# Performance work log

Hardware: AMD Instinct MI355X
Metric: run time of the kernel (lower is better)

Reference implementation:

```python
import jax, jax.numpy as jnp
import numpy as np

D_MODEL = 1024
N_HEADS = 16
HEAD_DIM = D_MODEL // N_HEADS  # 64
WINDOW = 15
NUM_RANDOM = 2
B, L = 2, 2048


def setup_inputs() -> dict:
    key = jax.random.key(0)
    ks = jax.random.split(key, 5)
    x = jax.random.normal(ks[0], (B, L, D_MODEL), dtype=jnp.float32)
    # rotary angles: theta[t, j] = t / 10000^(2j/head_dim), shape [1, L, head_dim//2]
    inv_freq = 1.0 / (10000.0 ** (jnp.arange(0, HEAD_DIM, 2, dtype=jnp.float32) / HEAD_DIM))
    t = jnp.arange(L, dtype=jnp.float32)
    freqs = (t[:, None] * inv_freq[None, :])[None].astype(jnp.float32)  # [1,L,32]
    scale = 0.02
    wq = jax.random.normal(ks[1], (D_MODEL, D_MODEL), dtype=jnp.float32) * scale
    wk = jax.random.normal(ks[2], (D_MODEL, D_MODEL), dtype=jnp.float32) * scale
    wv = jax.random.normal(ks[3], (D_MODEL, D_MODEL), dtype=jnp.float32) * scale
    wo = jax.random.normal(ks[4], (D_MODEL, D_MODEL), dtype=jnp.float32) * scale
    return {"x": x, "freqs": freqs, "wq": wq, "wk": wk, "wv": wv, "wo": wo}


def _rope(t, cos, sin):
    # t: [B,H,L,hd]; interpret last dim as (hd/2, 2) complex pairs and rotate.
    tr = t.reshape(*t.shape[:-1], -1, 2)
    re, im = tr[..., 0], tr[..., 1]
    out_re = re * cos - im * sin
    out_im = re * sin + im * cos
    return jnp.stack([out_re, out_im], axis=-1).reshape(t.shape)


def _bigbird_mask(Lq):
    ii = jnp.arange(Lq)[:, None]
    jj = jnp.arange(Lq)[None, :]
    causal = jj <= ii
    window = jnp.abs(ii - jj) <= (WINDOW // 2)
    glob = (ii == 0) | (jj == 0)
    # random mask: per row i, NUM_RANDOM indices uniform in [0, i]
    rkey = jax.random.key(42)
    u = jax.random.uniform(rkey, (Lq, NUM_RANDOM))
    ridx = jnp.floor(u * (jnp.arange(Lq, dtype=jnp.float32)[:, None] + 1.0)).astype(jnp.int32)
    rmask = jnp.zeros((Lq, Lq), dtype=bool).at[jnp.arange(Lq)[:, None], ridx].set(True)
    # rows with <= NUM_RANDOM causal options attend to all of them
    rmask = rmask | (causal & (ii < NUM_RANDOM))
    return (causal & (window | rmask)) | glob  # [L,L]


def reference(x, freqs, wq, wk, wv, wo):
    b, l, _ = x.shape
    q = (x @ wq.T).reshape(b, l, N_HEADS, HEAD_DIM).transpose(0, 2, 1, 3)  # [B,H,L,hd]
    k = (x @ wk.T).reshape(b, l, N_HEADS, HEAD_DIM).transpose(0, 2, 1, 3)
    v = (x @ wv.T).reshape(b, l, N_HEADS, HEAD_DIM).transpose(0, 2, 1, 3)
    cos = jnp.cos(freqs[:, :l])[:, None]  # [1,1,L,hd/2]
    sin = jnp.sin(freqs[:, :l])[:, None]
    q = _rope(q, cos, sin)
    k = _rope(k, cos, sin)
    attn_mask = _bigbird_mask(l)  # [L,L], broadcast over B,H
    scale = 1.0 / jnp.sqrt(jnp.float32(HEAD_DIM))
    scores = jnp.einsum("bhqd,bhkd->bhqk", q, k) * scale
    scores = jnp.where(attn_mask[None, None], scores, jnp.finfo(scores.dtype).min)
    p = jax.nn.softmax(scores, axis=-1)
    out = jnp.einsum("bhqk,bhkd->bhqd", p, v)
    out = out.transpose(0, 2, 1, 3).reshape(b, l, D_MODEL)
    return out @ wo.T
```

## Files before the change

kernel.cpp:

```cpp
#include <hip/hip_runtime.h>
#include <math.h>

#define SEQ_L 2048
#define DM 1024
#define NH 16
#define HD 64
#define NB 2
#define KD 1024
#define ND 1024

typedef __bf16 bf16;
typedef __bf16 bf16x8 __attribute__((ext_vector_type(8)));
typedef __bf16 bf16x4 __attribute__((ext_vector_type(4)));
typedef float f32x4 __attribute__((ext_vector_type(4)));

__device__ inline uint32_t rotl32(uint32_t v, int n) { return (v << n) | (v >> (32 - n)); }

__device__ inline void threefry(uint32_t x0, uint32_t x1, uint32_t* o0, uint32_t* o1) {
  const uint32_t ks0 = 0u, ks1 = 42u, ks2 = 0u ^ 42u ^ 0x1BD11BDAu;
  x0 += ks0; x1 += ks1;
#define TF_R(rr) { x0 += x1; x1 = rotl32(x1, rr); x1 ^= x0; }
  TF_R(13) TF_R(15) TF_R(26) TF_R(6)
  x0 += ks1; x1 += ks2 + 1u;
  TF_R(17) TF_R(29) TF_R(16) TF_R(24)
  x0 += ks2; x1 += ks0 + 2u;
  TF_R(13) TF_R(15) TF_R(26) TF_R(6)
  x0 += ks0; x1 += ks1 + 3u;
  TF_R(17) TF_R(29) TF_R(16) TF_R(24)
  x0 += ks1; x1 += ks2 + 4u;
  TF_R(13) TF_R(15) TF_R(26) TF_R(6)
  x0 += ks2; x1 += ks0 + 5u;
#undef TF_R
  *o0 = x0; *o1 = x1;
}

__device__ inline int rand_col(int i, int s) {
  uint32_t o0, o1;
  threefry(0u, (uint32_t)(2 * i + s), &o0, &o1);
  uint32_t bits = o0 ^ o1;
  float u = __uint_as_float((bits >> 9) | 0x3f800000u) - 1.0f;
  return (int)floorf(u * (float)(i + 1));
}

__global__ void prep_kernel(const float* __restrict__ x,
                            const float* __restrict__ w0, const float* __restrict__ w1,
                            const float* __restrict__ w2, const float* __restrict__ w3,
                            const float* __restrict__ freqs,
                            bf16* __restrict__ xb,
                            bf16* __restrict__ o0, bf16* __restrict__ o1,
                            bf16* __restrict__ o2, bf16* __restrict__ o3,
                            int* __restrict__ ctab, float2* __restrict__ rtab) {
  const int bx = blockIdx.x;
  const int t = threadIdx.x;
  if (bx < 8192) {
    const float* src;
    bf16* dst;
    int idx;
    if (bx < 4096) { src = x; dst = xb; idx = bx * 256 + t; }
    else {
      int widx = bx - 4096;
      int wsel = widx >> 10;
      switch (wsel) {
        case 0: src = w0; dst = o0; break;
        case 1: src = w1; dst = o1; break;
        case 2: src = w2; dst = o2; break;
        default: src = w3; dst = o3; break;
      }
      idx = (widx & 1023) * 256 + t;
    }
    float4 vv = ((const float4*)src)[idx];
    bf16x4 ov;
    ov[0] = (bf16)vv.x; ov[1] = (bf16)vv.y; ov[2] = (bf16)vv.z; ov[3] = (bf16)vv.w;
    *(bf16x4*)(dst + (size_t)idx * 4) = ov;
    return;
  }
  if (bx < 8200) {
    const int i = (bx - 8192) * 256 + t;
    int cols[11]; int nc = 0;
    if (i >= 1) {
      int lo = i - 7; if (lo < 0) lo = 0;
      for (int j = lo; j <= i; ++j) cols[nc++] = j;
      if (lo > 0) cols[nc++] = 0;
#pragma unroll
      for (int s = 0; s < 2; ++s) {
        int rj = rand_col(i, s);
        bool dup = false;
        for (int c2 = 0; c2 < nc; ++c2) dup |= (cols[c2] == rj);
        if (!dup) cols[nc++] = rj;
      }
    }
    for (int c2 = nc; c2 < 11; ++c2) cols[c2] = -1;
#pragma unroll
    for (int c2 = 0; c2 < 11; ++c2) ctab[i * 12 + c2] = cols[c2];
    ctab[i * 12 + 11] = nc;
    return;
  }
  const int idx = (bx - 8200) * 256 + t;
  float s, c;
  sincosf(freqs[idx], &s, &c);
  rtab[idx] = make_float2(c, s);
}

__device__ inline void gld16(const bf16* g, bf16* l) {
  __builtin_amdgcn_global_load_lds((const __attribute__((address_space(1))) void*)g,
                                   (__attribute__((address_space(3))) void*)l, 16, 0, 0);
}

template <typename OutT>
__device__ inline void gemm_bt_body(const bf16* __restrict__ A, const bf16* __restrict__ W,
                                    OutT* __restrict__ C, const float2* __restrict__ rtab) {
  __shared__ __align__(16) bf16 As[128 * 32];
  __shared__ __align__(16) bf16 Bs[128 * 32];
  const int t = threadIdx.x;
  const int lane = t & 63;
  const int wave = t >> 6;
  const int wm = (wave >> 1) * 64;
  const int wn = (wave & 1) * 64;
  const int m0 = blockIdx.x * 128;
  const int n0 = blockIdx.y * 128;
  const int r = t >> 2;
  const int ck = (t & 3) * 8;
  const int l15 = lane & 15;
  const int koff = (lane >> 4) * 8;

  f32x4 acc[4][4] = {};

  for (int k0 = 0; k0 < KD; k0 += 32) {
    gld16(A + (size_t)(m0 + r) * KD + k0 + ck, As + t * 8);
    gld16(A + (size_t)(m0 + 64 + r) * KD + k0 + ck, As + 2048 + t * 8);
    gld16(W + (size_t)(n0 + r) * KD + k0 + ck, Bs + t * 8);
    gld16(W + (size_t)(n0 + 64 + r) * KD + k0 + ck, Bs + 2048 + t * 8);
    __syncthreads();
    bf16x8 af[4], bfr[4];
#pragma unroll
    for (int mt = 0; mt < 4; ++mt)
      af[mt] = *(const bf16x8*)(As + (wm + mt * 16 + l15) * 32 + koff);
#pragma unroll
    for (int nt = 0; nt < 4; ++nt)
      bfr[nt] = *(const bf16x8*)(Bs + (wn + nt * 16 + l15) * 32 + koff);
#pragma unroll
    for (int mt = 0; mt < 4; ++mt)
#pragma unroll
      for (int nt = 0; nt < 4; ++nt)
        acc[mt][nt] = __builtin_amdgcn_mfma_f32_16x16x32_bf16(af[mt], bfr[nt], acc[mt][nt], 0, 0, 0);
    __syncthreads();
  }
  const int colb = n0 + wn + l15;
  const int rowb = m0 + wm + (lane >> 4) * 4;
  const int odd = l15 & 1;
#pragma unroll
  for (int mt = 0; mt < 4; ++mt)
#pragma unroll
    for (int nt = 0; nt < 4; ++nt) {
      const int col = colb + nt * 16;
      const int jj = (col & 63) >> 1;
#pragma unroll
      for (int rr = 0; rr < 4; ++rr) {
        float val = acc[mt][nt][rr];
        if (rtab) {
          const int row = rowb + mt * 16 + rr;
          const int l = row & (SEQ_L - 1);
          float2 cs = rtab[l * 32 + jj];
          float partner = __shfl_xor(val, 1);
          val = odd ? val * cs.x + partner * cs.y : val * cs.x - partner * cs.y;
        }
        C[(size_t)(rowb + mt * 16 + rr) * ND + colb + nt * 16] = (OutT)val;
      }
    }
}

__global__ __launch_bounds__(256, 3) void qkv_gemm_kernel(
    const bf16* __restrict__ xb, const bf16* __restrict__ wqb, const bf16* __restrict__ wkb,
    const bf16* __restrict__ wvb, bf16* __restrict__ qb, bf16* __restrict__ kb, bf16* __restrict__ vb,
    const float2* __restrict__ rtab) {
  const bf16* W = blockIdx.z == 0 ? wqb : blockIdx.z == 1 ? wkb : wvb;
  bf16* O = blockIdx.z == 0 ? qb : blockIdx.z == 1 ? kb : vb;
  const float2* rt = blockIdx.z < 2 ? rtab : nullptr;
  gemm_bt_body<bf16>(xb, W, O, rt);
}

__global__ __launch_bounds__(256, 2) void out_gemm_kernel(
    bf16* __restrict__ ab, const bf16* __restrict__ wob, float* __restrict__ out,
    const float* __restrict__ pm, const float* __restrict__ pz, const float* __restrict__ pv) {
  const int t = threadIdx.x;
  const int m0 = blockIdx.x * 64;
  const int n0 = blockIdx.y * 128;

  if (blockIdx.x == 0 || blockIdx.x == 32) {
    const int b = blockIdx.x == 0 ? 0 : 1;
#pragma unroll
    for (int e = t; e < DM; e += 256) {
      const int h = e >> 6, d = e & 63;
      const int base = b * 128 + h * 8;
      float M = -1e30f;
#pragma unroll
      for (int c = 0; c < 8; ++c) M = fmaxf(M, pm[base + c]);
      float Z = 0.f, od = 0.f;
#pragma unroll
      for (int c = 0; c < 8; ++c) {
        float sc = __expf(pm[base + c] - M);
        Z += pz[base + c] * sc;
        od += pv[(base + c) * 64 + d] * sc;
      }
      ab[(size_t)b * SEQ_L * DM + e] = (bf16)(od / Z);
    }
    __syncthreads();
  }

  __shared__ __align__(16) bf16 As[64 * 32];
  __shared__ __align__(16) bf16 Bs[128 * 32];
  const int lane = t & 63;
  const int wave = t >> 6;
  const int wm = (wave >> 1) * 32;
  const int wn = (wave & 1) * 64;
  const int r = t >> 2;
  const int ck = (t & 3) * 8;
  const int l15 = lane & 15;
  const int koff = (lane >> 4) * 8;

  f32x4 acc[2][4] = {};

  for (int k0 = 0; k0 < KD; k0 += 32) {
    gld16(ab + (size_t)(m0 + r) * KD + k0 + ck, As + t * 8);
    gld16(wob + (size_t)(n0 + r) * KD + k0 + ck, Bs + t * 8);
    gld16(wob + (size_t)(n0 + 64 + r) * KD + k0 + ck, Bs + 2048 + t * 8);
    __syncthreads();
    bf16x8 af[2], bfr[4];
#pragma unroll
    for (int mt = 0; mt < 2; ++mt)
      af[mt] = *(const bf16x8*)(As + (wm + mt * 16 + l15) * 32 + koff);
#pragma unroll
    for (int nt = 0; nt < 4; ++nt)
      bfr[nt] = *(const bf16x8*)(Bs + (wn + nt * 16 + l15) * 32 + koff);
#pragma unroll
    for (int mt = 0; mt < 2; ++mt)
#pragma unroll
      for (int nt = 0; nt < 4; ++nt)
        acc[mt][nt] = __builtin_amdgcn_mfma_f32_16x16x32_bf16(af[mt], bfr[nt], acc[mt][nt], 0, 0, 0);
    __syncthreads();
  }
  const int colb = n0 + wn + l15;
  const int rowb = m0 + wm + (lane >> 4) * 4;
#pragma unroll
  for (int mt = 0; mt < 2; ++mt)
#pragma unroll
    for (int nt = 0; nt < 4; ++nt)
#pragma unroll
      for (int rr = 0; rr < 4; ++rr)
        out[(size_t)(rowb + mt * 16 + rr) * ND + colb + nt * 16] = acc[mt][nt][rr];
}

__global__ __launch_bounds__(256) void attn_kernel(const bf16* __restrict__ q, const bf16* __restrict__ k,
                                                   const bf16* __restrict__ v, bf16* __restrict__ o,
                                                   const int* __restrict__ ctab,
                                                   float* __restrict__ pm, float* __restrict__ pz,
                                                   float* __restrict__ pv) {
  const int t = threadIdx.x;
  const int lane = t & 63;
  const int w = t >> 6;

  __shared__ float sbuf[256];
  __shared__ float redm[4], redz[4];
  __shared__ float part[4][64];

  if (blockIdx.x < 1024) {
    const int b = blockIdx.x >> 9;
    const int tt = blockIdx.x & 511;
    const int tile = ((tt & 7) << 6) + (tt >> 3);
    const int i = tile * 4 + 1 + w;
    if (i >= SEQ_L) return;
    const size_t bb = (size_t)b * SEQ_L * DM;
    const int eo = lane * 16;

    const bf16* qrow = q + bb + (size_t)i * DM + eo;
    bf16x8 qv0 = *(const bf16x8*)(qrow);
    bf16x8 qv1 = *(const bf16x8*)(qrow + 8);

    const int4* cp = (const int4*)(ctab + i * 12);
    int4 ca = cp[0], cb = cp[1], cc = cp[2];
    int cols[11] = {ca.x, ca.y, ca.z, ca.w, cb.x, cb.y, cb.z, cb.w, cc.x, cc.y, cc.z};

    float sv[11];
#pragma unroll
    for (int c = 0; c < 11; ++c) {
      int cj = cols[c] < 0 ? 0 : cols[c];
      const bf16* krow = k + bb + (size_t)cj * DM + eo;
      bf16x8 kv0 = *(const bf16x8*)(krow);
      bf16x8 kv1 = *(const bf16x8*)(krow + 8);
      float acc = 0.f;
#pragma unroll
      for (int e = 0; e < 8; ++e)
        acc += (float)qv0[e] * (float)kv0[e] + (float)qv1[e] * (float)kv1[e];
      sv[c] = acc;
    }
#pragma unroll
    for (int c = 0; c < 11; ++c) {
      sv[c] += __shfl_xor(sv[c], 1);
      sv[c] += __shfl_xor(sv[c], 2);
      sv[c] = cols[c] < 0 ? -1e30f : sv[c] * 0.125f;
    }
    float m = -1e30f;
#pragma unroll
    for (int c = 0; c < 11; ++c) m = fmaxf(m, sv[c]);
    float z = 0.f;
#pragma unroll
    for (int c = 0; c < 11; ++c) { sv[c] = __expf(sv[c] - m); z += sv[c]; }
    const float inv = 1.f / z;

    float oa[16] = {};
#pragma unroll
    for (int c = 0; c < 11; ++c) {
      int cj = cols[c] < 0 ? 0 : cols[c];
      const bf16* vrow = v + bb + (size_t)cj * DM + eo;
      bf16x8 vv0 = *(const bf16x8*)(vrow);
      bf16x8 vv1 = *(const bf16x8*)(vrow + 8);
#pragma unroll
      for (int e = 0; e < 8; ++e) {
        oa[e]     += sv[c] * (float)vv0[e];
        oa[8 + e] += sv[c] * (float)vv1[e];
      }
    }
    bf16x8 ov0, ov1;
#pragma unroll
    for (int e = 0; e < 8; ++e) {
      ov0[e] = (bf16)(oa[e] * inv);
      ov1[e] = (bf16)(oa[8 + e] * inv);
    }
    bf16* orow = o + bb + (size_t)i * DM + eo;
    *(bf16x8*)(orow) = ov0;
    *(bf16x8*)(orow + 8) = ov1;
    return;
  }

  const int idx = blockIdx.x - 1024;
  const int b = idx >> 7;
  const int rem = idx & 127;
  const int h = rem >> 3;
  const int c = rem & 7;
  const size_t hb = (size_t)b * SEQ_L * DM + (size_t)h * HD;
  const int j = c * 256 + t;

  bf16x8 qv8[8];
#pragma unroll
  for (int cc = 0; cc < 8; ++cc) qv8[cc] = *(const bf16x8*)(q + hb + cc * 8);

  float acc = 0.f;
#pragma unroll
  for (int cc = 0; cc < 8; ++cc) {
    bf16x8 kv = *(const bf16x8*)(k + hb + (size_t)j * DM + cc * 8);
#pragma unroll
    for (int e = 0; e < 8; ++e) acc += (float)qv8[cc][e] * (float)kv[e];
  }
  float s = acc * 0.125f;
  float mloc = s;
#pragma unroll
  for (int off = 32; off > 0; off >>= 1) mloc = fmaxf(mloc, __shfl_xor(mloc, off));
  if (lane == 0) redm[w] = mloc;
  __syncthreads();
  const float m = fmaxf(fmaxf(redm[0], redm[1]), fmaxf(redm[2], redm[3]));

  float e = __expf(s - m);
  sbuf[t] = e;
  float zloc = e;
#pragma unroll
  for (int off = 32; off > 0; off >>= 1) zloc += __shfl_xor(zloc, off);
  if (lane == 0) redz[w] = zloc;
  __syncthreads();
  const float zc = redz[0] + redz[1] + redz[2] + redz[3];

  float oa = 0.f;
  for (int jj = w; jj < 256; jj += 4)
    oa += sbuf[jj] * (float)v[hb + (size_t)(c * 256 + jj) * DM + lane];
  part[w][lane] = oa;
  __syncthreads();
  if (t < 64) pv[idx * 64 + t] = part[0][t] + part[1][t] + part[2][t] + part[3][t];
  if (t == 0) { pm[idx] = m; pz[idx] = zc; }
}

extern "C" void kernel_launch(void* const* d_in, const int* in_sizes, int n_in,
                              void* d_out, int out_size, void* d_ws, size_t ws_size,
                              hipStream_t stream) {
  const float* x     = (const float*)d_in[0];
  const float* freqs = (const float*)d_in[1];
  const float* wq    = (const float*)d_in[2];
  const float* wk    = (const float*)d_in[3];
  const float* wv    = (const float*)d_in[4];
  const float* wo    = (const float*)d_in[5];
  float* out = (float*)d_out;

  char* ws = (char*)d_ws;
  bf16* xb  = (bf16*)(ws + 0);
  bf16* wqb = (bf16*)(ws + 8388608);
  bf16* wkb = (bf16*)(ws + 10485760);
  bf16* wvb = (bf16*)(ws + 12582912);
  bf16* wob = (bf16*)(ws + 14680064);
  bf16* qb  = (bf16*)(ws + 16777216);
  bf16* kb  = (bf16*)(ws + 25165824);
  bf16* vb  = (bf16*)(ws + 33554432);
  bf16* ab  = (bf16*)(ws + 41943040);
  int*    ctab = (int*)(ws + 50331648);
  float*  pm   = (float*)(ws + 50462720);
  float*  pz   = (float*)(ws + 50463744);
  float*  pv   = (float*)(ws + 50464768);
  float2* rtab = (float2*)(ws + 50593792);
  (void)ws_size;

  prep_kernel<<<8456, 256, 0, stream>>>(x, wq, wk, wv, wo, freqs, xb, wqb, wkb, wvb, wob, ctab, rtab);
  qkv_gemm_kernel<<<dim3(32, 8, 3), 256, 0, stream>>>(xb, wqb, wkb, wvb, qb, kb, vb, rtab);
  attn_kernel<<<dim3(1280, 1), 256, 0, stream>>>(qb, kb, vb, ab, ctab, pm, pz, pv);
  out_gemm_kernel<<<dim3(64, 8), 256, 0, stream>>>(ab, wob, out, pm, pz, pv);
}
```

Before: 173.8 us.

## Double GEMM K-tile to 64 with XOR-swizzled LDS and paired bf16 stores

Both the QKV and output GEMMs now stage a 64-wide K slice per iteration instead of 32. This halves the number of barrier pairs per GEMM. The LDS layout is XOR-swizzled per row so that the 128-byte row stride does not cause bank conflicts on MFMA fragment reads. The QKV epilogue now has even lanes apply RoPE and write two adjacent bf16 values as one packed store, replacing per-element stores. The larger tiles double LDS use per block, which may reduce occupancy.

```diff
diff --git a/kernel.cpp b/kernel.cpp
--- a/kernel.cpp
+++ b/kernel.cpp
@@ -12,6 +12,7 @@
 typedef __bf16 bf16;
 typedef __bf16 bf16x8 __attribute__((ext_vector_type(8)));
 typedef __bf16 bf16x4 __attribute__((ext_vector_type(4)));
+typedef __bf16 bf16x2 __attribute__((ext_vector_type(2)));
 typedef float f32x4 __attribute__((ext_vector_type(4)));
 
 __device__ inline uint32_t rotl32(uint32_t v, int n) { return (v << n) | (v >> (32 - n)); }
@@ -106,11 +107,10 @@
                                    (__attribute__((address_space(3))) void*)l, 16, 0, 0);
 }
 
-template <typename OutT>
 __device__ inline void gemm_bt_body(const bf16* __restrict__ A, const bf16* __restrict__ W,
-                                    OutT* __restrict__ C, const float2* __restrict__ rtab) {
-  __shared__ __align__(16) bf16 As[128 * 32];
-  __shared__ __align__(16) bf16 Bs[128 * 32];
+                                    bf16* __restrict__ C, const float2* __restrict__ rtab) {
+  __shared__ __align__(16) bf16 As[128 * 64];
+  __shared__ __align__(16) bf16 Bs[128 * 64];
   const int t = threadIdx.x;
   const int lane = t & 63;
   const int wave = t >> 6;
@@ -118,31 +118,41 @@
   const int wn = (wave & 1) * 64;
   const int m0 = blockIdx.x * 128;
   const int n0 = blockIdx.y * 128;
-  const int r = t >> 2;
-  const int ck = (t & 3) * 8;
   const int l15 = lane & 15;
-  const int koff = (lane >> 4) * 8;
+  const int kq = lane >> 4;
 
   f32x4 acc[4][4] = {};
 
-  for (int k0 = 0; k0 < KD; k0 += 32) {
-    gld16(A + (size_t)(m0 + r) * KD + k0 + ck, As + t * 8);
-    gld16(A + (size_t)(m0 + 64 + r) * KD + k0 + ck, As + 2048 + t * 8);
-    gld16(W + (size_t)(n0 + r) * KD + k0 + ck, Bs + t * 8);
-    gld16(W + (size_t)(n0 + 64 + r) * KD + k0 + ck, Bs + 2048 + t * 8);
+  for (int k0 = 0; k0 < KD; k0 += 64) {
+#pragma unroll
+    for (int n = 0; n < 4; ++n) {
+      const int s = n * 256 + t;
+      const int row = s >> 3;
+      const int ch = (s & 7) ^ (row & 7);
+      gld16(A + (size_t)(m0 + row) * KD + k0 + ch * 8, As + s * 8);
+      gld16(W + (size_t)(n0 + row) * KD + k0 + ch * 8, Bs + s * 8);
+    }
     __syncthreads();
-    bf16x8 af[4], bfr[4];
-#pragma unroll
-    for (int mt = 0; mt < 4; ++mt)
-      af[mt] = *(const bf16x8*)(As + (wm + mt * 16 + l15) * 32 + koff);
-#pragma unroll
-    for (int nt = 0; nt < 4; ++nt)
-      bfr[nt] = *(const bf16x8*)(Bs + (wn + nt * 16 + l15) * 32 + koff);
-#pragma unroll
-    for (int mt = 0; mt < 4; ++mt)
-#pragma unroll
-      for (int nt = 0; nt < 4; ++nt)
-        acc[mt][nt] = __builtin_amdgcn_mfma_f32_16x16x32_bf16(af[mt], bfr[nt], acc[mt][nt], 0, 0, 0);
+#pragma unroll
+    for (int ks = 0; ks < 2; ++ks) {
+      const int cb = ks * 4 + kq;
+      bf16x8 af[4], bfr[4];
+#pragma unroll
+      for (int mt = 0; mt < 4; ++mt) {
+        const int row = wm + mt * 16 + l15;
+        af[mt] = *(const bf16x8*)(As + row * 64 + ((cb ^ (row & 7)) * 8));
+      }
+#pragma unroll
+      for (int nt = 0; nt < 4; ++nt) {
+        const int row = wn + nt * 16 + l15;
+        bfr[nt] = *(const bf16x8*)(Bs + row * 64 + ((cb ^ (row & 7)) * 8));
+      }
+#pragma unroll
+      for (int mt = 0; mt < 4; ++mt)
+#pragma unroll
+        for (int nt = 0; nt < 4; ++nt)
+          acc[mt][nt] = __builtin_amdgcn_mfma_f32_16x16x32_bf16(af[mt], bfr[nt], acc[mt][nt], 0, 0, 0);
+    }
     __syncthreads();
   }
   const int colb = n0 + wn + l15;
@@ -157,14 +167,18 @@
 #pragma unroll
       for (int rr = 0; rr < 4; ++rr) {
         float val = acc[mt][nt][rr];
-        if (rtab) {
+        float other = __shfl_xor(val, 1);
+        if (!odd) {
           const int row = rowb + mt * 16 + rr;
-          const int l = row & (SEQ_L - 1);
-          float2 cs = rtab[l * 32 + jj];
-          float partner = __shfl_xor(val, 1);
-          val = odd ? val * cs.x + partner * cs.y : val * cs.x - partner * cs.y;
+          float lo, hi;
+          if (rtab) {
+            float2 cs = rtab[(row & (SEQ_L - 1)) * 32 + jj];
+            lo = val * cs.x - other * cs.y;
+            hi = val * cs.y + other * cs.x;
+          } else { lo = val; hi = other; }
+          bf16x2 p; p[0] = (bf16)lo; p[1] = (bf16)hi;
+          *(bf16x2*)(C + (size_t)row * ND + col) = p;
         }
-        C[(size_t)(rowb + mt * 16 + rr) * ND + colb + nt * 16] = (OutT)val;
       }
     }
 }
@@ -176,7 +190,7 @@
   const bf16* W = blockIdx.z == 0 ? wqb : blockIdx.z == 1 ? wkb : wvb;
   bf16* O = blockIdx.z == 0 ? qb : blockIdx.z == 1 ? kb : vb;
   const float2* rt = blockIdx.z < 2 ? rtab : nullptr;
-  gemm_bt_body<bf16>(xb, W, O, rt);
+  gemm_bt_body(xb, W, O, rt);
 }
 
 __global__ __launch_bounds__(256, 2) void out_gemm_kernel(
@@ -207,36 +221,53 @@
     __syncthreads();
   }
 
-  __shared__ __align__(16) bf16 As[64 * 32];
-  __shared__ __align__(16) bf16 Bs[128 * 32];
+  __shared__ __align__(16) bf16 As[64 * 64];
+  __shared__ __align__(16) bf16 Bs[128 * 64];
   const int lane = t & 63;
   const int wave = t >> 6;
   const int wm = (wave >> 1) * 32;
   const int wn = (wave & 1) * 64;
-  const int r = t >> 2;
-  const int ck = (t & 3) * 8;
   const int l15 = lane & 15;
-  const int koff = (lane >> 4) * 8;
+  const int kq = lane >> 4;
 
   f32x4 acc[2][4] = {};
 
-  for (int k0 = 0; k0 < KD; k0 += 32) {
-    gld16(ab + (size_t)(m0 + r) * KD + k0 + ck, As + t * 8);
-    gld16(wob + (size_t)(n0 + r) * KD + k0 + ck, Bs + t * 8);
-    gld16(wob + (size_t)(n0 + 64 + r) * KD + k0 + ck, Bs + 2048 + t * 8);
+  for (int k0 = 0; k0 < KD; k0 += 64) {
+#pragma unroll
+    for (int n = 0; n < 2; ++n) {
+      const int s = n * 256 + t;
+      const int row = s >> 3;
+      const int ch = (s & 7) ^ (row & 7);
+      gld16(ab + (size_t)(m0 + row) * KD + k0 + ch * 8, As + s * 8);
+    }
+#pragma unroll
+    for (int n = 0; n < 4; ++n) {
+      const int s = n * 256 + t;
+      const int row = s >> 3;
+      const int ch = (s & 7) ^ (row & 7);
+      gld16(wob + (size_t)(n0 + row) * KD + k0 + ch * 8, Bs + s * 8);
+    }
     __syncthreads();
-    bf16x8 af[2], bfr[4];
-#pragma unroll
-    for (int mt = 0; mt < 2; ++mt)
-      af[mt] = *(const bf16x8*)(As + (wm + mt * 16 + l15) * 32 + koff);
-#pragma unroll
-    for (int nt = 0; nt < 4; ++nt)
-      bfr[nt] = *(const bf16x8*)(Bs + (wn + nt * 16 + l15) * 32 + koff);
-#pragma unroll
-    for (int mt = 0; mt < 2; ++mt)
-#pragma unroll
-      for (int nt = 0; nt < 4; ++nt)
-        acc[mt][nt] = __builtin_amdgcn_mfma_f32_16x16x32_bf16(af[mt], bfr[nt], acc[mt][nt], 0, 0, 0);
+#pragma unroll
+    for (int ks = 0; ks < 2; ++ks) {
+      const int cb = ks * 4 + kq;
+      bf16x8 af[2], bfr[4];
+#pragma unroll
+      for (int mt = 0; mt < 2; ++mt) {
+        const int row = wm + mt * 16 + l15;
+        af[mt] = *(const bf16x8*)(As + row * 64 + ((cb ^ (row & 7)) * 8));
+      }
+#pragma unroll
+      for (int nt = 0; nt < 4; ++nt) {
+        const int row = wn + nt * 16 + l15;
+        bfr[nt] = *(const bf16x8*)(Bs + row * 64 + ((cb ^ (row & 7)) * 8));
+      }
+#pragma unroll
+      for (int mt = 0; mt < 2; ++mt)
+#pragma unroll
+        for (int nt = 0; nt < 4; ++nt)
+          acc[mt][nt] = __builtin_amdgcn_mfma_f32_16x16x32_bf16(af[mt], bfr[nt], acc[mt][nt], 0, 0, 0);
+    }
     __syncthreads();
   }
   const int colb = n0 + wn + l15;
```

Measured after the change: 170.9 us. Within noise of the previous version (-1.6%).
